# Optimization experiments

Measured on AMD Instinct MI355X. Metric: run time of the kernel, lower is better.

The kernel has to match this reference:

```python
import jax, jax.numpy as jnp
import numpy as np

C = 256
RED = 2
C2 = C // RED


def setup_inputs() -> dict:
    key = jax.random.key(0)
    ks = jax.random.split(key, 6)
    B, H, W = 8, 64, 64
    x = jax.random.normal(ks[0], (B, C, H, W), dtype=jnp.float32)
    # 1x1 convs stored as [out_ch, in_ch] matrices
    W1 = jax.random.normal(ks[1], (C2, C), dtype=jnp.float32) * (1.0 / np.sqrt(C))
    b1 = jax.random.normal(ks[2], (C2,), dtype=jnp.float32) * 0.01
    W2 = jax.random.normal(ks[3], (C, C2), dtype=jnp.float32) * (1.0 / np.sqrt(C2))
    b2 = jax.random.normal(ks[4], (C,), dtype=jnp.float32) * 0.01
    # torch inits scale to zeros; use randn so the residual branch is active
    scale = jax.random.normal(ks[5], (1, C, 1, 1), dtype=jnp.float32)
    return {"x": x, "W1": W1, "b1": b1, "W2": W2, "b2": b2, "scale": scale}


def reference(x, W1, b1, W2, b2, scale):
    B, Cc, H, Wd = x.shape
    # conv1 (1x1): [B,C,H,W] -> [B,C2,H,W]
    y = jnp.einsum('bchw,oc->bohw', x, W1) + b1[None, :, None, None]
    # flatten spatial, move channels last: [B, N, C2]
    y = y.reshape(B, C2, H * Wd).transpose(0, 2, 1)
    # unscaled self-attention over N spatial positions
    att = jax.nn.softmax(jnp.einsum('bmc,bnc->bmn', y, y), axis=-1)  # [B,N,N]
    out = jnp.einsum('bmn,bnc->bmc', att, y)  # [B,N,C2]
    # faithful to torch: raw .view(B,-1,H,W) WITHOUT permuting back
    out = out.reshape(B, C2, H, Wd)
    # conv2 (1x1): [B,C2,H,W] -> [B,C,H,W]
    out = jnp.einsum('bchw,oc->bohw', out, W2) + b2[None, :, None, None]
    return out * scale + x
```

## Files before the change

### kernel.cpp

```cpp
#include <hip/hip_runtime.h>

#define B_  8
#define C_  256
#define C2_ 128
#define N_  4096
#define LOG2E 1.44269504088896f

typedef _Float16 f16;
typedef _Float16 f16x4 __attribute__((ext_vector_type(4)));
typedef _Float16 f16x8 __attribute__((ext_vector_type(8)));
typedef float f32x4  __attribute__((ext_vector_type(4)));

__global__ __launch_bounds__(256)
void prep_kernel(const float* __restrict__ W1, const float* __restrict__ W2,
                 f16* __restrict__ w1h, f16* __restrict__ w2h)
{
  int i = blockIdx.x * 256 + threadIdx.x;
  w1h[i] = (f16)W1[i];
  w2h[i] = (f16)W2[i];
}

__global__ __launch_bounds__(256, 3)
void conv1_kernel(const float* __restrict__ x,
                  const f16* __restrict__ w1h,
                  const float* __restrict__ b1,
                  f16* __restrict__ Y, f16* __restrict__ Yt)
{
  __shared__ __align__(16) char smem[49152];
  float* Xr = (float*)smem;
  f16*   Ah = (f16*)(smem + 32768);
  f16*   T  = (f16*)smem;

  const int t = threadIdx.x;
  const int w = t >> 6, lane = t & 63, quad = lane >> 4, l16 = lane & 15;
  const int b = blockIdx.x, nt0 = blockIdx.y;

#pragma unroll
  for (int pass = 0; pass < 8; pass++) {
    int c  = (t >> 3) + pass * 32;
    int n4 = t & 7;
    float4 v = *(const float4*)(x + ((long)(b * C_ + c)) * N_ + nt0 * 32 + n4 * 4);
    *(float4*)(&Xr[c * 32 + (n4 ^ (c & 7)) * 4]) = v;
  }
  __syncthreads();
#pragma unroll
  for (int pass = 0; pass < 4; pass++) {
    int n  = t & 31;
    int kb = (t >> 5) + pass * 8;
    f16x8 vh;
#pragma unroll
    for (int jj = 0; jj < 8; jj++) {
      int cc = kb * 8 + jj;
      vh[jj] = (f16)Xr[cc * 32 + ((n >> 2) ^ (cc & 7)) * 4 + (n & 3)];
    }
    *(f16x8*)(&Ah[n * 256 + (kb ^ (n & 7)) * 8]) = vh;
  }
  __syncthreads();

  f16x8 bh[2][8];
#pragma unroll
  for (int nt = 0; nt < 2; nt++) {
    int c2 = w * 32 + nt * 16 + l16;
#pragma unroll
    for (int ks = 0; ks < 8; ks++)
      bh[nt][ks] = *(const f16x8*)(w1h + c2 * C_ + ks * 32 + quad * 8);
  }

  f32x4 acc[2][2];
#pragma unroll
  for (int i = 0; i < 2; i++)
#pragma unroll
    for (int j = 0; j < 2; j++) acc[i][j] = (f32x4){0.f, 0.f, 0.f, 0.f};

#pragma unroll
  for (int ks = 0; ks < 8; ks++)
#pragma unroll
    for (int mt = 0; mt < 2; mt++) {
      f16x8 ah = *(const f16x8*)(&Ah[(mt * 16 + l16) * 256 + (((ks * 4 + quad) ^ (l16 & 7))) * 8]);
#pragma unroll
      for (int nt = 0; nt < 2; nt++)
        acc[mt][nt] = __builtin_amdgcn_mfma_f32_16x16x32_f16(ah, bh[nt][ks], acc[mt][nt], 0, 0, 0);
    }
  __syncthreads();

#pragma unroll
  for (int nt = 0; nt < 2; nt++) {
    int c2 = w * 32 + nt * 16 + l16;
    float bv = b1[c2];
#pragma unroll
    for (int mt = 0; mt < 2; mt++)
#pragma unroll
      for (int rg = 0; rg < 4; rg++) {
        int n = mt * 16 + quad * 4 + rg;
        T[c2 * 40 + n] = (f16)(acc[mt][nt][rg] + bv);
      }
  }
  __syncthreads();
#pragma unroll
  for (int pass = 0; pass < 2; pass++) {
    int r  = (t >> 2) + pass * 64;
    int c8 = (t & 3) * 8;
    f16x8 v = *(const f16x8*)(&T[r * 40 + c8]);
    *(f16x8*)(Yt + ((long)(b * C2_ + r)) * N_ + nt0 * 32 + c8) = v;
  }
#pragma unroll
  for (int pass = 0; pass < 2; pass++) {
    int row = t & 31;
    int cg  = (t >> 5) + pass * 8;
    f16x8 v;
#pragma unroll
    for (int jj = 0; jj < 8; jj++) v[jj] = T[(cg * 8 + jj) * 40 + row];
    *(f16x8*)(Y + ((long)(b * N_ + nt0 * 32 + row)) * C2_ + cg * 8) = v;
  }
}

__global__ __launch_bounds__(256, 2)
void attn_kernel(const f16* __restrict__ Y, const f16* __restrict__ Yt,
                 f16* __restrict__ Op, float* __restrict__ ls)
{
  __shared__ f16 Ks[64 * 128];
  __shared__ f16 Vs[128 * 64];
  __shared__ float nsqf[128];

  const int t = threadIdx.x;
  const int w = t >> 6, lane = t & 63, quad = lane >> 4, l16 = lane & 15;
  const int b = blockIdx.x, qt = blockIdx.y, s = blockIdx.z;
  const f16* Yb  = Y  + (long)b * N_ * C2_;
  const f16* Ytb = Yt + (long)b * C2_ * N_;
  const int kbase0 = s * 2048;

  f16x8 qf[2][4];
#pragma unroll
  for (int mt = 0; mt < 2; mt++)
#pragma unroll
    for (int ks = 0; ks < 4; ks++)
      qf[mt][ks] = *(const f16x8*)(Yb + (long)(qt * 128 + w * 32 + mt * 16 + l16) * C2_ + ks * 32 + quad * 8);

  {
    int r = t >> 1, half = t & 1;
    float ss = 0.f;
#pragma unroll
    for (int j = 0; j < 8; j++) {
      f16x8 v = *(const f16x8*)(Yb + (long)(qt * 128 + r) * C2_ + half * 64 + j * 8);
#pragma unroll
      for (int e = 0; e < 8; e++) { float f = (float)v[e]; ss = fmaf(f, f, ss); }
    }
    ss += __shfl_xor(ss, 1);
    if (!half) nsqf[r] = ss;
  }

#pragma unroll
  for (int pass = 0; pass < 4; pass++) {
    int r = (t >> 4) + pass * 16;
    f16x8 kv = *(const f16x8*)(Yb + (long)(kbase0 + r) * C2_ + (t & 15) * 8);
    *(f16x8*)(&Ks[r * 128 + (((t & 15)) ^ (r & 15)) * 8]) = kv;
  }
#pragma unroll
  for (int pass = 0; pass < 4; pass++) {
    int d = (t >> 3) + pass * 32;
    f16x8 vv = *(const f16x8*)(Ytb + (long)d * N_ + kbase0 + (t & 7) * 8);
    *(f16x8*)(&Vs[d * 64 + (((t & 7)) ^ (d & 7)) * 8]) = vv;
  }
  __syncthreads();

  float nm[2];
  nm[0] = nsqf[w * 32 + l16] * LOG2E;
  nm[1] = nsqf[w * 32 + 16 + l16] * LOG2E;

  const f16x4 ones4 = {(f16)1.f, (f16)1.f, (f16)1.f, (f16)1.f};

  f32x4 Oa[2][8];
#pragma unroll
  for (int i = 0; i < 2; i++)
#pragma unroll
    for (int j = 0; j < 8; j++) Oa[i][j] = (f32x4){0.f, 0.f, 0.f, 0.f};
  f32x4 lac[2] = {(f32x4){0.f,0.f,0.f,0.f}, (f32x4){0.f,0.f,0.f,0.f}};

#pragma unroll 1
  for (int kt = 0; kt < 32; kt++) {
    f16x8 stK[4], stV[4];
    if (kt + 1 < 32) {
      int nb = kbase0 + (kt + 1) * 64;
#pragma unroll
      for (int pass = 0; pass < 4; pass++)
        stK[pass] = *(const f16x8*)(Yb + (long)(nb + (t >> 4) + pass * 16) * C2_ + (t & 15) * 8);
#pragma unroll
      for (int pass = 0; pass < 4; pass++)
        stV[pass] = *(const f16x8*)(Ytb + (long)((t >> 3) + pass * 32) * N_ + nb + (t & 7) * 8);
    }

    f32x4 S[4][2];
#pragma unroll
    for (int i = 0; i < 4; i++)
#pragma unroll
      for (int j = 0; j < 2; j++) S[i][j] = (f32x4){0.f, 0.f, 0.f, 0.f};
#pragma unroll
    for (int ks = 0; ks < 4; ks++) {
      f16x8 bfr[4];
#pragma unroll
      for (int nt = 0; nt < 4; nt++)
        bfr[nt] = *(const f16x8*)(&Ks[(nt * 16 + l16) * 128 + (((ks * 4 + quad) ^ l16)) * 8]);
#pragma unroll
      for (int nt = 0; nt < 4; nt++)
#pragma unroll
        for (int mt = 0; mt < 2; mt++)
          S[nt][mt] = __builtin_amdgcn_mfma_f32_16x16x32_f16(bfr[nt], qf[mt][ks], S[nt][mt], 0, 0, 0);
    }

    f16x4 pb[4][2];
#pragma unroll
    for (int nt = 0; nt < 4; nt++)
#pragma unroll
      for (int mt = 0; mt < 2; mt++) {
        f16x4 pv;
#pragma unroll
        for (int rg = 0; rg < 4; rg++)
          pv[rg] = (f16)exp2f(fminf(fmaf(S[nt][mt][rg], LOG2E, -nm[mt]), 11.0f));
        pb[nt][mt] = pv;
      }

#pragma unroll
    for (int nt = 0; nt < 4; nt++)
#pragma unroll
      for (int mt = 0; mt < 2; mt++)
        lac[mt] = __builtin_amdgcn_mfma_f32_16x16x16f16(ones4, pb[nt][mt], lac[mt], 0, 0, 0);

#pragma unroll
    for (int nt = 0; nt < 4; nt++) {
#pragma unroll
      for (int dt = 0; dt < 8; dt++) {
        f16x4 va = *(const f16x4*)(&Vs[(dt * 16 + l16) * 64
                      + (((nt * 2 + (quad >> 1)) ^ (l16 & 7))) * 8 + (quad & 1) * 4]);
#pragma unroll
        for (int mt = 0; mt < 2; mt++)
          Oa[mt][dt] = __builtin_amdgcn_mfma_f32_16x16x16f16(va, pb[nt][mt], Oa[mt][dt], 0, 0, 0);
      }
    }

    __syncthreads();
    if (kt + 1 < 32) {
#pragma unroll
      for (int pass = 0; pass < 4; pass++) {
        int r = (t >> 4) + pass * 16;
        *(f16x8*)(&Ks[r * 128 + (((t & 15)) ^ (r & 15)) * 8]) = stK[pass];
      }
#pragma unroll
      for (int pass = 0; pass < 4; pass++) {
        int d = (t >> 3) + pass * 32;
        *(f16x8*)(&Vs[d * 64 + (((t & 7)) ^ (d & 7)) * 8]) = stV[pass];
      }
    }
    __syncthreads();
  }

  const long rbase = ((long)s * B_ + b) * N_ + qt * 128;
#pragma unroll
  for (int mt = 0; mt < 2; mt++) {
    int q = w * 32 + mt * 16 + l16;
#pragma unroll
    for (int dt = 0; dt < 8; dt++) {
      f16x4 ov = {(f16)Oa[mt][dt][0], (f16)Oa[mt][dt][1],
                  (f16)Oa[mt][dt][2], (f16)Oa[mt][dt][3]};
      *(f16x4*)(Op + (rbase + q) * C2_ + dt * 16 + quad * 4) = ov;
    }
    if (quad == 0) ls[rbase + q] = lac[mt][0];
  }
}

__global__ __launch_bounds__(256, 4)
void conv2_kernel(const f16* __restrict__ Op, const float* __restrict__ ls,
                  const f16* __restrict__ w2h,
                  const float* __restrict__ b2,
                  const float* __restrict__ scale,
                  const float* __restrict__ x,
                  float* __restrict__ out)
{
  __shared__ f16 Or[128 * 72];
  __shared__ f16 Bsw[64 * 128];
  __shared__ float invL[128];

  const int t = threadIdx.x;
  const int w = t >> 6, lane = t & 63, quad = lane >> 4, l16 = lane & 15;
  const int b = blockIdx.x, pt = blockIdx.y, oh = blockIdx.z;
  const long base0 = (long)b * 524288;
  const long base1 = 4194304 + base0;

  if (t < 128) {
    int q = t * 32 + (pt >> 1);
    float l = ls[(long)b * N_ + q] + ls[32768 + (long)b * N_ + q];
    invL[t] = 1.0f / fmaxf(l, 1e-20f);
  }
  __syncthreads();

#pragma unroll
  for (int pass = 0; pass < 4; pass++) {
    int j = (t >> 3) + pass * 32;
    int c8 = (t & 7) * 8;
    f16x8 a0 = *(const f16x8*)(Op + base0 + (long)j * N_ + pt * 64 + c8);
    f16x8 a1 = *(const f16x8*)(Op + base1 + (long)j * N_ + pt * 64 + c8);
    float iv = invL[j];
    f16x8 r;
#pragma unroll
    for (int jj = 0; jj < 8; jj++)
      r[jj] = (f16)(((float)a0[jj] + (float)a1[jj]) * iv);
    *(f16x8*)(&Or[j * 72 + c8]) = r;
  }
  __syncthreads();
#pragma unroll
  for (int pass = 0; pass < 4; pass++) {
    int p = t & 63;
    int q = (t >> 6) + pass * 4;
    f16x8 vv;
#pragma unroll
    for (int jj = 0; jj < 8; jj++) vv[jj] = Or[(q * 8 + jj) * 72 + p];
    *(f16x8*)(&Bsw[p * 128 + ((q ^ (p & 15))) * 8]) = vv;
  }
  __syncthreads();

  f32x4 acc[2][4];
#pragma unroll
  for (int i = 0; i < 2; i++)
#pragma unroll
    for (int j = 0; j < 4; j++) acc[i][j] = (f32x4){0.f, 0.f, 0.f, 0.f};

#pragma unroll
  for (int ks = 0; ks < 4; ks++) {
    f16x8 bfr[4];
#pragma unroll
    for (int nt = 0; nt < 4; nt++)
      bfr[nt] = *(const f16x8*)(&Bsw[(nt * 16 + l16) * 128 + (((ks * 4 + quad) ^ l16)) * 8]);
#pragma unroll
    for (int mt = 0; mt < 2; mt++) {
      int o = oh * 128 + w * 32 + mt * 16 + l16;
      f16x8 ah = *(const f16x8*)(w2h + o * C2_ + ks * 32 + quad * 8);
#pragma unroll
      for (int nt = 0; nt < 4; nt++)
        acc[mt][nt] = __builtin_amdgcn_mfma_f32_16x16x32_f16(ah, bfr[nt], acc[mt][nt], 0, 0, 0);
    }
  }
#pragma unroll
  for (int mt = 0; mt < 2; mt++)
#pragma unroll
    for (int rg = 0; rg < 4; rg++) {
      int o = oh * 128 + w * 32 + mt * 16 + quad * 4 + rg;
      float so = scale[o], bo = b2[o];
#pragma unroll
      for (int nt = 0; nt < 4; nt++) {
        int p = pt * 64 + nt * 16 + l16;
        long xo = ((long)b * C_ + o) * N_ + p;
        out[xo] = (acc[mt][nt][rg] + bo) * so + x[xo];
      }
    }
}

extern "C" void kernel_launch(void* const* d_in, const int* in_sizes, int n_in,
                              void* d_out, int out_size, void* d_ws, size_t ws_size,
                              hipStream_t stream) {
  const float* x     = (const float*)d_in[0];
  const float* W1    = (const float*)d_in[1];
  const float* b1    = (const float*)d_in[2];
  const float* W2    = (const float*)d_in[3];
  const float* b2    = (const float*)d_in[4];
  const float* scale = (const float*)d_in[5];
  float* outp = (float*)d_out;

  const size_t NE = (size_t)B_ * N_ * C2_;
  f16* Y   = (f16*)d_ws;
  f16* Yt  = Y + NE;
  f16* Op  = Yt + NE;
  float* ls = (float*)(Op + 2 * NE);
  f16* w1h = (f16*)(ls + 65536);
  f16* w2h = w1h + 32768;

  prep_kernel <<<dim3(128),      dim3(256), 0, stream>>>(W1, W2, w1h, w2h);
  conv1_kernel<<<dim3(8, 128),   dim3(256), 0, stream>>>(x, w1h, b1, Y, Yt);
  attn_kernel <<<dim3(8, 32, 2), dim3(256), 0, stream>>>(Y, Yt, Op, ls);
  conv2_kernel<<<dim3(8, 64, 2), dim3(256), 0, stream>>>(Op, ls, w2h, b2, scale, x, outp);
}
```

Baseline: 225.5 us.

## Use 16x16x32 MFMA for PV product via in-register P layout shuffle

The P·V product and row-sum accumulation switch from 16x16x16 MFMAs with P as the B operand to 16x16x32 MFMAs with P as the A operand. The P tile is repacked across lanes with permlane32_swap and ds_swizzle so that it matches the A-operand layout. V is now read from LDS as 8-wide fragments. This halves the number of MFMA issues and widens the LDS reads, at the cost of extra cross-lane shuffle instructions. The output store becomes transposed scalar f16 writes, which are less vectorized.

```diff
diff --git a/kernel.cpp b/kernel.cpp
--- a/kernel.cpp
+++ b/kernel.cpp
@@ -7,9 +7,14 @@
 #define LOG2E 1.44269504088896f
 
 typedef _Float16 f16;
-typedef _Float16 f16x4 __attribute__((ext_vector_type(4)));
+typedef _Float16 f16x2 __attribute__((ext_vector_type(2)));
 typedef _Float16 f16x8 __attribute__((ext_vector_type(8)));
 typedef float f32x4  __attribute__((ext_vector_type(4)));
+
+static __device__ __forceinline__ unsigned pk2(float a, float b) {
+  f16x2 h = {(f16)a, (f16)b};
+  return __builtin_bit_cast(unsigned, h);
+}
 
 __global__ __launch_bounds__(256)
 void prep_kernel(const float* __restrict__ W1, const float* __restrict__ W2,
@@ -167,7 +172,9 @@
   nm[0] = nsqf[w * 32 + l16] * LOG2E;
   nm[1] = nsqf[w * 32 + 16 + l16] * LOG2E;
 
-  const f16x4 ones4 = {(f16)1.f, (f16)1.f, (f16)1.f, (f16)1.f};
+  f16x8 ones8;
+#pragma unroll
+  for (int j = 0; j < 8; j++) ones8[j] = (f16)1.0f;
 
   f32x4 Oa[2][8];
 #pragma unroll
@@ -207,33 +214,62 @@
           S[nt][mt] = __builtin_amdgcn_mfma_f32_16x16x32_f16(bfr[nt], qf[mt][ks], S[nt][mt], 0, 0, 0);
     }
 
-    f16x4 pb[4][2];
-#pragma unroll
-    for (int nt = 0; nt < 4; nt++)
+    unsigned Xp[2][4][2];
+#pragma unroll
+    for (int mt = 0; mt < 2; mt++)
+#pragma unroll
+      for (int nt = 0; nt < 4; nt++) {
+        float p0 = exp2f(fminf(fmaf(S[nt][mt][0], LOG2E, -nm[mt]), 11.0f));
+        float p1 = exp2f(fminf(fmaf(S[nt][mt][1], LOG2E, -nm[mt]), 11.0f));
+        float p2 = exp2f(fminf(fmaf(S[nt][mt][2], LOG2E, -nm[mt]), 11.0f));
+        float p3 = exp2f(fminf(fmaf(S[nt][mt][3], LOG2E, -nm[mt]), 11.0f));
+        Xp[mt][nt][0] = pk2(p0, p1);
+        Xp[mt][nt][1] = pk2(p2, p3);
+      }
+
+    f16x8 pa[2][2];
+    {
+      const bool par = (quad & 1) != 0;
 #pragma unroll
       for (int mt = 0; mt < 2; mt++) {
-        f16x4 pv;
-#pragma unroll
-        for (int rg = 0; rg < 4; rg++)
-          pv[rg] = (f16)exp2f(fminf(fmaf(S[nt][mt][rg], LOG2E, -nm[mt]), 11.0f));
-        pb[nt][mt] = pv;
-      }
-
-#pragma unroll
-    for (int nt = 0; nt < 4; nt++)
-#pragma unroll
-      for (int mt = 0; mt < 2; mt++)
-        lac[mt] = __builtin_amdgcn_mfma_f32_16x16x16f16(ones4, pb[nt][mt], lac[mt], 0, 0, 0);
-
-#pragma unroll
-    for (int nt = 0; nt < 4; nt++) {
-#pragma unroll
-      for (int dt = 0; dt < 8; dt++) {
-        f16x4 va = *(const f16x4*)(&Vs[(dt * 16 + l16) * 64
-                      + (((nt * 2 + (quad >> 1)) ^ (l16 & 7))) * 8 + (quad & 1) * 4]);
-#pragma unroll
-        for (int mt = 0; mt < 2; mt++)
-          Oa[mt][dt] = __builtin_amdgcn_mfma_f32_16x16x16f16(va, pb[nt][mt], Oa[mt][dt], 0, 0, 0);
+#pragma unroll
+        for (int pr = 0; pr < 2; pr++)
+#pragma unroll
+          for (int d = 0; d < 2; d++) {
+            auto r = __builtin_amdgcn_permlane32_swap(Xp[mt][2 * pr][d], Xp[mt][2 * pr + 1][d], false, false);
+            Xp[mt][2 * pr][d]     = r[0];
+            Xp[mt][2 * pr + 1][d] = r[1];
+          }
+#pragma unroll
+        for (int ks2 = 0; ks2 < 2; ks2++) {
+          unsigned lo0 = Xp[mt][2 * ks2][0],     lo1 = Xp[mt][2 * ks2][1];
+          unsigned hi0 = Xp[mt][2 * ks2 + 1][0], hi1 = Xp[mt][2 * ks2 + 1][1];
+          unsigned lo0x = (unsigned)__builtin_amdgcn_ds_swizzle((int)lo0, 0x401F);
+          unsigned lo1x = (unsigned)__builtin_amdgcn_ds_swizzle((int)lo1, 0x401F);
+          unsigned hi0x = (unsigned)__builtin_amdgcn_ds_swizzle((int)hi0, 0x401F);
+          unsigned hi1x = (unsigned)__builtin_amdgcn_ds_swizzle((int)hi1, 0x401F);
+          union { unsigned u[4]; f16x8 v; } P;
+          P.u[0] = par ? hi0x : lo0;
+          P.u[1] = par ? hi1x : lo1;
+          P.u[2] = par ? hi0  : lo0x;
+          P.u[3] = par ? hi1  : lo1x;
+          pa[ks2][mt] = P.v;
+        }
+      }
+    }
+
+#pragma unroll
+    for (int ks2 = 0; ks2 < 2; ks2++) {
+      f16x8 vb[8];
+#pragma unroll
+      for (int dt = 0; dt < 8; dt++)
+        vb[dt] = *(const f16x8*)(&Vs[(dt * 16 + l16) * 64 + (((ks2 * 4 + quad) ^ (l16 & 7))) * 8]);
+#pragma unroll
+      for (int mt = 0; mt < 2; mt++) {
+#pragma unroll
+        for (int dt = 0; dt < 8; dt++)
+          Oa[mt][dt] = __builtin_amdgcn_mfma_f32_16x16x32_f16(pa[ks2][mt], vb[dt], Oa[mt][dt], 0, 0, 0);
+        lac[mt] = __builtin_amdgcn_mfma_f32_16x16x32_f16(pa[ks2][mt], ones8, lac[mt], 0, 0, 0);
       }
     }
 
@@ -255,16 +291,15 @@
 
   const long rbase = ((long)s * B_ + b) * N_ + qt * 128;
 #pragma unroll
-  for (int mt = 0; mt < 2; mt++) {
-    int q = w * 32 + mt * 16 + l16;
-#pragma unroll
-    for (int dt = 0; dt < 8; dt++) {
-      f16x4 ov = {(f16)Oa[mt][dt][0], (f16)Oa[mt][dt][1],
-                  (f16)Oa[mt][dt][2], (f16)Oa[mt][dt][3]};
-      *(f16x4*)(Op + (rbase + q) * C2_ + dt * 16 + quad * 4) = ov;
-    }
-    if (quad == 0) ls[rbase + q] = lac[mt][0];
-  }
+  for (int mt = 0; mt < 2; mt++)
+#pragma unroll
+    for (int rg = 0; rg < 4; rg++) {
+      int r = w * 32 + mt * 16 + quad * 4 + rg;
+#pragma unroll
+      for (int dt = 0; dt < 8; dt++)
+        Op[(rbase + r) * C2_ + dt * 16 + l16] = (f16)Oa[mt][dt][rg];
+      if (l16 == 0) ls[rbase + r] = lac[mt][rg];
+    }
 }
 
 __global__ __launch_bounds__(256, 4)
```

Result: faster. 213.1 us (-5.5%).
